# Kernel optimization log

Measured on AMD Instinct MI355X. Metric: run time of the kernel, lower is better.

## Reference

```python
import jax, jax.numpy as jnp
import numpy as np

T, H, I, E, K = 1024, 2048, 1408, 8, 2  # tokens, hidden, moe_intermediate, n_experts, top_k

def setup_inputs() -> dict:
    key = jax.random.key(0)
    k0, k1, k2, k3 = jax.random.split(key, 4)
    def w(k, shape, fan_in):
        return jax.random.normal(k, shape, jnp.float32) / np.float32(np.sqrt(fan_in))
    return {
        "hidden_states": jax.random.normal(k0, (T, H), jnp.float32),
        "gate_w": w(k1, (H, E), H),      # router: LiteLinear(H -> E), no bias
        "w1": w(k2, (E, H, I), H),        # experts_w1 [E, H, I]
        "w2": w(k3, (E, I, H), I),        # experts_w2 [E, I, H]
    }

def reference(hidden_states, gate_w, w1, w2):
    # Router: logits -> softmax -> top-k expert probabilities (no renorm; Qwen2MoE norm_topk_prob=False)
    router_logits = hidden_states @ gate_w                      # [T, E]
    probs = jax.nn.softmax(router_logits, axis=-1)              # [T, E]
    topk_vals, topk_idx = jax.lax.top_k(probs, K)               # [T, K]
    # Dense combine weights: zero except at the top-k experts of each token
    combine = jnp.sum(jax.nn.one_hot(topk_idx, E, dtype=probs.dtype) * topk_vals[..., None], axis=1)  # [T, E]
    # Expert MLP per source: down(silu(x @ w1)) — note: no gate/up split in this repo's fused_moe weights
    h = jnp.einsum('th,ehi->tei', hidden_states, w1)            # [T, E, I]
    y = jnp.einsum('tei,eih->teh', jax.nn.silu(h), w2)          # [T, E, H]
    return jnp.einsum('te,teh->th', combine, y)                 # [T, H]
```

## Files before the change

kernel.cpp:

```cpp
#include <hip/hip_runtime.h>
#include <hip/hip_fp16.h>

#define T_TOK 1024
#define H_DIM 2048
#define I_DIM 1408
#define N_EXP 8
#define TOPK  2

using f16x8 = __attribute__((ext_vector_type(8))) _Float16;
using f32x4 = __attribute__((ext_vector_type(4))) float;

#define BM 128
#define BN 64
#define BK 64
#define NTHR 512
#define MBLKS 8

#define WS_COUNTS      0
#define WS_BASES       256
#define WS_CURSORS     512
#define WS_TOPK_E      768
#define WS_TOPK_W      (768 + 8192)
#define WS_TOK_OF_SLOT 17408
#define WS_W_OF_SLOT   29696
#define WS_HACT        43008
#define WS_NEEDED      (43008 + 8650752)

__global__ void k_router(const float* __restrict__ X, const float* __restrict__ GW,
                         int* __restrict__ counts, int* __restrict__ topk_e,
                         float* __restrict__ topk_w) {
    int t = (blockIdx.x * blockDim.x + threadIdx.x) >> 6;
    int lane = threadIdx.x & 63;
    if (t >= T_TOK) return;
    float acc[N_EXP];
#pragma unroll
    for (int e = 0; e < N_EXP; ++e) acc[e] = 0.f;
    const float* xrow = X + (size_t)t * H_DIM;
    for (int h = lane; h < H_DIM; h += 64) {
        float x = xrow[h];
        const float* g = GW + (size_t)h * N_EXP;
#pragma unroll
        for (int e = 0; e < N_EXP; ++e) acc[e] = fmaf(x, g[e], acc[e]);
    }
#pragma unroll
    for (int off = 32; off > 0; off >>= 1) {
#pragma unroll
        for (int e = 0; e < N_EXP; ++e) acc[e] += __shfl_xor(acc[e], off, 64);
    }
    if (lane == 0) {
        float m = acc[0];
#pragma unroll
        for (int e = 1; e < N_EXP; ++e) m = fmaxf(m, acc[e]);
        float ex[N_EXP], s = 0.f;
#pragma unroll
        for (int e = 0; e < N_EXP; ++e) { ex[e] = expf(acc[e] - m); s += ex[e]; }
        float inv = 1.f / s;
        int e1 = 0;
#pragma unroll
        for (int e = 1; e < N_EXP; ++e) if (ex[e] > ex[e1]) e1 = e;
        int e2 = (e1 == 0) ? 1 : 0;
#pragma unroll
        for (int e = 0; e < N_EXP; ++e) if (e != e1 && ex[e] > ex[e2]) e2 = e;
        topk_e[t * 2 + 0] = e1;
        topk_e[t * 2 + 1] = e2;
        topk_w[t * 2 + 0] = ex[e1] * inv;
        topk_w[t * 2 + 1] = ex[e2] * inv;
        atomicAdd(&counts[e1], 1);
        atomicAdd(&counts[e2], 1);
    }
}

__global__ void k_prefix(const int* __restrict__ counts, int* __restrict__ bases,
                         int* __restrict__ cursors) {
    if (threadIdx.x == 0) {
        int b = 0;
        for (int e = 0; e < N_EXP; ++e) {
            bases[e] = b;
            b += ((counts[e] + BM - 1) / BM) * BM;
            cursors[e] = 0;
        }
    }
}

__global__ void k_scatter(const int* __restrict__ topk_e, const float* __restrict__ topk_w,
                          const int* __restrict__ bases, int* __restrict__ cursors,
                          int* __restrict__ tok_of_slot, float* __restrict__ w_of_slot) {
    int t = blockIdx.x * blockDim.x + threadIdx.x;
    if (t >= T_TOK) return;
    for (int j = 0; j < TOPK; ++j) {
        int e = topk_e[t * 2 + j];
        int pos = atomicAdd(&cursors[e], 1);
        int slot = bases[e] + pos;
        tok_of_slot[slot] = t;
        w_of_slot[slot] = topk_w[t * 2 + j];
    }
}


#define G_COMPUTE(buf)                                                          \
    do {                                                                        \
        _Pragma("unroll") for (int ks = 0; ks < 2; ++ks) {                      \
            f16x8 af[2], bf[2];                                                 \
            _Pragma("unroll") for (int ii = 0; ii < 2; ++ii) {                  \
                int r = wm + ii * 16 + rsel;                                    \
                af[ii] = *(const f16x8*)&As[buf][r][((kq + 4 * ks) ^ (r & 7)) * 8]; \
            }                                                                   \
            _Pragma("unroll") for (int jj = 0; jj < 2; ++jj) {                  \
                int r = wn + jj * 16 + rsel;                                    \
                bf[jj] = *(const f16x8*)&Bs[buf][r][((kq + 4 * ks) ^ (r & 7)) * 8]; \
            }                                                                   \
            _Pragma("unroll") for (int ii = 0; ii < 2; ++ii)                    \
                _Pragma("unroll") for (int jj = 0; jj < 2; ++jj)                \
                    acc[ii][jj] = __builtin_amdgcn_mfma_f32_16x16x32_f16(af[ii], bf[jj], acc[ii][jj], 0, 0, 0); \
        }                                                                       \
    } while (0)

#define G_DECODE(NB)                                \
    const int bi = blockIdx.x;                      \
    const int xcd = bi & 7;                         \
    const int kk = bi >> 3;                         \
    const int mblk = kk & (MBLKS - 1);              \
    const int P = xcd + 8 * (kk / MBLKS);           \
    const int e = P / (NB);                         \
    const int n = P % (NB);

__global__ __launch_bounds__(NTHR, 4) void k_gemm1(
    const float* __restrict__ X, const float* __restrict__ W1,
    const int* __restrict__ counts, const int* __restrict__ bases,
    const int* __restrict__ tok_of_slot, const float* __restrict__ w_of_slot,
    _Float16* __restrict__ hact) {
    __shared__ _Float16 As[2][BM][BK];
    __shared__ _Float16 Bs[2][BN][BK];

    G_DECODE(I_DIM / BN)
    const int cnt = counts[e];
    const int m0 = mblk * BM;
    if (m0 >= cnt) return;
    const int base = bases[e];
    const int n0 = n * BN;
    const int tid = threadIdx.x;

    const int ar = tid >> 2;
    const int ac2 = (tid & 3) * 2;
    const int r_eff = min(ar, cnt - m0 - 1);
    const float* arow = X + (size_t)tok_of_slot[base + m0 + r_eff] * H_DIM + (tid & 3) * 16;

    const int bn = tid & 63;
    const int bc = tid >> 6;
    const float* bcol = W1 + (size_t)e * (H_DIM * I_DIM) + (size_t)(bc * 8) * I_DIM + n0 + bn;

    const int wid = tid >> 6, lane = tid & 63;
    const int wm = (wid >> 1) * 32, wn = (wid & 1) * 32;
    const int rsel = lane & 15, kq = lane >> 4;

    f32x4 acc[2][2] = {};

    float4 aR0[4]; float bR0[8];
    float4 aR1[4]; float bR1[8];

#define LOAD1(aR, bR, k0)                                              \
    do {                                                               \
        aR[0] = *(const float4*)(arow + (k0));                         \
        aR[1] = *(const float4*)(arow + (k0) + 4);                     \
        aR[2] = *(const float4*)(arow + (k0) + 8);                     \
        aR[3] = *(const float4*)(arow + (k0) + 12);                    \
        const float* bp = bcol + (size_t)(k0) * I_DIM;                 \
        _Pragma("unroll") for (int j = 0; j < 8; ++j)                  \
            bR[j] = bp[(size_t)j * I_DIM];                             \
    } while (0)

#define STORE1(buf, aR, bR)                                            \
    do {                                                               \
        f16x8 p0, p1;                                                  \
        _Pragma("unroll") for (int j = 0; j < 4; ++j) {                \
            p0[j]     = (_Float16)aR[0][j];                            \
            p0[j + 4] = (_Float16)aR[1][j];                            \
            p1[j]     = (_Float16)aR[2][j];                            \
            p1[j + 4] = (_Float16)aR[3][j];                            \
        }                                                              \
        *(f16x8*)&As[buf][ar][((ac2) ^ (ar & 7)) * 8] = p0;            \
        *(f16x8*)&As[buf][ar][((ac2 + 1) ^ (ar & 7)) * 8] = p1;        \
        f16x8 q;                                                       \
        _Pragma("unroll") for (int j = 0; j < 8; ++j)                  \
            q[j] = (_Float16)bR[j];                                    \
        *(f16x8*)&Bs[buf][bn][(bc ^ (bn & 7)) * 8] = q;                \
    } while (0)

    const int KT = H_DIM / BK;
    LOAD1(aR0, bR0, 0);
    STORE1(0, aR0, bR0);
    LOAD1(aR0, bR0, BK);
    __syncthreads();
    for (int kt = 0; kt < KT; kt += 2) {
        if (kt + 2 < KT) LOAD1(aR1, bR1, (kt + 2) * BK);
        G_COMPUTE(0);
        if (kt + 1 < KT) STORE1(1, aR0, bR0);
        __syncthreads();
        if (kt + 3 < KT) LOAD1(aR0, bR0, (kt + 3) * BK);
        if (kt + 1 < KT) {
            G_COMPUTE(1);
            if (kt + 2 < KT) STORE1(0, aR1, bR1);
            __syncthreads();
        }
    }
#undef LOAD1
#undef STORE1

    const int rows = cnt - m0;
#pragma unroll
    for (int i = 0; i < 2; ++i) {
#pragma unroll
        for (int rg = 0; rg < 4; ++rg) {
            int r = wm + i * 16 + kq * 4 + rg;
            if (r < rows) {
                int slot = base + m0 + r;
                float w = w_of_slot[slot];
                _Float16* hrow = hact + (size_t)slot * I_DIM + n0;
#pragma unroll
                for (int j = 0; j < 2; ++j) {
                    float v = acc[i][j][rg];
                    hrow[wn + j * 16 + rsel] = (_Float16)(v / (1.f + expf(-v)) * w);
                }
            }
        }
    }
}

__global__ __launch_bounds__(NTHR, 4) void k_gemm2(
    const _Float16* __restrict__ hact, const float* __restrict__ W2,
    const int* __restrict__ counts, const int* __restrict__ bases,
    const int* __restrict__ tok_of_slot, float* __restrict__ out) {
    __shared__ _Float16 As[2][BM][BK];
    __shared__ _Float16 Bs[2][BN][BK];

    G_DECODE(H_DIM / BN)
    const int cnt = counts[e];
    const int m0 = mblk * BM;
    if (m0 >= cnt) return;
    const int base = bases[e];
    const int n0 = n * BN;
    const int tid = threadIdx.x;

    const int ar = tid >> 2;
    const int ac2 = (tid & 3) * 2;
    const int r_eff = min(ar, cnt - m0 - 1);
    const _Float16* arow = hact + (size_t)(base + m0 + r_eff) * I_DIM + (tid & 3) * 16;

    const int bn = tid & 63;
    const int bc = tid >> 6;
    const float* bcol = W2 + (size_t)e * (I_DIM * H_DIM) + (size_t)(bc * 8) * H_DIM + n0 + bn;

    const int wid = tid >> 6, lane = tid & 63;
    const int wm = (wid >> 1) * 32, wn = (wid & 1) * 32;
    const int rsel = lane & 15, kq = lane >> 4;

    f32x4 acc[2][2] = {};

    f16x8 aR0[2]; float bR0[8];
    f16x8 aR1[2]; float bR1[8];

#define LOAD2(aR, bR, k0)                                              \
    do {                                                               \
        aR[0] = *(const f16x8*)(arow + (k0));                          \
        aR[1] = *(const f16x8*)(arow + (k0) + 8);                      \
        const float* bp = bcol + (size_t)(k0) * H_DIM;                 \
        _Pragma("unroll") for (int j = 0; j < 8; ++j)                  \
            bR[j] = bp[(size_t)j * H_DIM];                             \
    } while (0)

#define STORE2(buf, aR, bR)                                            \
    do {                                                               \
        *(f16x8*)&As[buf][ar][((ac2) ^ (ar & 7)) * 8] = aR[0];         \
        *(f16x8*)&As[buf][ar][((ac2 + 1) ^ (ar & 7)) * 8] = aR[1];     \
        f16x8 q;                                                       \
        _Pragma("unroll") for (int j = 0; j < 8; ++j)                  \
            q[j] = (_Float16)bR[j];                                    \
        *(f16x8*)&Bs[buf][bn][(bc ^ (bn & 7)) * 8] = q;                \
    } while (0)

    const int KT = I_DIM / BK;
    LOAD2(aR0, bR0, 0);
    STORE2(0, aR0, bR0);
    LOAD2(aR0, bR0, BK);
    __syncthreads();
    for (int kt = 0; kt < KT; kt += 2) {
        if (kt + 2 < KT) LOAD2(aR1, bR1, (kt + 2) * BK);
        G_COMPUTE(0);
        if (kt + 1 < KT) STORE2(1, aR0, bR0);
        __syncthreads();
        if (kt + 3 < KT) LOAD2(aR0, bR0, (kt + 3) * BK);
        if (kt + 1 < KT) {
            G_COMPUTE(1);
            if (kt + 2 < KT) STORE2(0, aR1, bR1);
            __syncthreads();
        }
    }
#undef LOAD2
#undef STORE2

    const int rows = cnt - m0;
#pragma unroll
    for (int i = 0; i < 2; ++i) {
#pragma unroll
        for (int rg = 0; rg < 4; ++rg) {
            int r = wm + i * 16 + kq * 4 + rg;
            if (r < rows) {
                int slot = base + m0 + r;
                int tok = tok_of_slot[slot];
                float* orow = out + (size_t)tok * H_DIM + n0;
#pragma unroll
                for (int j = 0; j < 2; ++j)
                    atomicAdd(&orow[wn + j * 16 + rsel], acc[i][j][rg]);
            }
        }
    }
}

extern "C" void kernel_launch(void* const* d_in, const int* in_sizes, int n_in,
                              void* d_out, int out_size, void* d_ws, size_t ws_size,
                              hipStream_t stream) {
    const float* X  = (const float*)d_in[0];
    const float* GW = (const float*)d_in[1];
    const float* W1 = (const float*)d_in[2];
    const float* W2 = (const float*)d_in[3];
    float* out = (float*)d_out;
    char* ws = (char*)d_ws;
    if (ws_size < (size_t)WS_NEEDED) return;

    int*   counts      = (int*)(ws + WS_COUNTS);
    int*   bases       = (int*)(ws + WS_BASES);
    int*   cursors     = (int*)(ws + WS_CURSORS);
    int*   topk_e      = (int*)(ws + WS_TOPK_E);
    float* topk_w      = (float*)(ws + WS_TOPK_W);
    int*   tok_of_slot = (int*)(ws + WS_TOK_OF_SLOT);
    float* w_of_slot   = (float*)(ws + WS_W_OF_SLOT);
    _Float16* hact     = (_Float16*)(ws + WS_HACT);

    hipMemsetAsync(counts, 0, N_EXP * sizeof(int), stream);
    k_router<<<T_TOK / 4, 256, 0, stream>>>(X, GW, counts, topk_e, topk_w);
    k_prefix<<<1, 64, 0, stream>>>(counts, bases, cursors);
    k_scatter<<<T_TOK / 256, 256, 0, stream>>>(topk_e, topk_w, bases, cursors,
                                               tok_of_slot, w_of_slot);
    hipMemsetAsync(out, 0, (size_t)T_TOK * H_DIM * sizeof(float), stream);
    k_gemm1<<<8 * MBLKS * 22, NTHR, 0, stream>>>(
        X, W1, counts, bases, tok_of_slot, w_of_slot, hact);
    k_gemm2<<<8 * MBLKS * 32, NTHR, 0, stream>>>(
        hact, W2, counts, bases, tok_of_slot, out);
}
```

Measured before the change: 184.6 us.

## Use plain 3D grid, lighter barriers, and earlier output memset

Replaces the XCD-aware swizzled 1D block decode with a straightforward 3D grid (n tiles, m tiles, expert). It also replaces __syncthreads with an explicit lgkmcnt wait plus s_barrier, and moves the output memset to before the router. The 3D grid changes which blocks share an XCD L2, so the same weight tiles may be reused less within each L2 slice. The lighter barrier avoids waiting on outstanding global loads (vmcnt) at each sync, which could let the prefetches overlap more with compute.

```diff
diff --git a/kernel.cpp b/kernel.cpp
--- a/kernel.cpp
+++ b/kernel.cpp
@@ -14,7 +14,12 @@
 #define BN 64
 #define BK 64
 #define NTHR 512
-#define MBLKS 8
+
+#define BAR()                                                     \
+    do {                                                          \
+        asm volatile("s_waitcnt lgkmcnt(0)" ::: "memory");        \
+        __builtin_amdgcn_s_barrier();                             \
+    } while (0)
 
 #define WS_COUNTS      0
 #define WS_BASES       256
@@ -115,15 +120,6 @@
         }                                                                       \
     } while (0)
 
-#define G_DECODE(NB)                                \
-    const int bi = blockIdx.x;                      \
-    const int xcd = bi & 7;                         \
-    const int kk = bi >> 3;                         \
-    const int mblk = kk & (MBLKS - 1);              \
-    const int P = xcd + 8 * (kk / MBLKS);           \
-    const int e = P / (NB);                         \
-    const int n = P % (NB);
-
 __global__ __launch_bounds__(NTHR, 4) void k_gemm1(
     const float* __restrict__ X, const float* __restrict__ W1,
     const int* __restrict__ counts, const int* __restrict__ bases,
@@ -132,12 +128,12 @@
     __shared__ _Float16 As[2][BM][BK];
     __shared__ _Float16 Bs[2][BN][BK];
 
-    G_DECODE(I_DIM / BN)
+    const int e = blockIdx.z;
     const int cnt = counts[e];
-    const int m0 = mblk * BM;
+    const int m0 = blockIdx.y * BM;
     if (m0 >= cnt) return;
     const int base = bases[e];
-    const int n0 = n * BN;
+    const int n0 = blockIdx.x * BN;
     const int tid = threadIdx.x;
 
     const int ar = tid >> 2;
@@ -190,17 +186,17 @@
     LOAD1(aR0, bR0, 0);
     STORE1(0, aR0, bR0);
     LOAD1(aR0, bR0, BK);
-    __syncthreads();
+    BAR();
     for (int kt = 0; kt < KT; kt += 2) {
         if (kt + 2 < KT) LOAD1(aR1, bR1, (kt + 2) * BK);
         G_COMPUTE(0);
         if (kt + 1 < KT) STORE1(1, aR0, bR0);
-        __syncthreads();
+        BAR();
         if (kt + 3 < KT) LOAD1(aR0, bR0, (kt + 3) * BK);
         if (kt + 1 < KT) {
             G_COMPUTE(1);
             if (kt + 2 < KT) STORE1(0, aR1, bR1);
-            __syncthreads();
+            BAR();
         }
     }
 #undef LOAD1
@@ -233,12 +229,12 @@
     __shared__ _Float16 As[2][BM][BK];
     __shared__ _Float16 Bs[2][BN][BK];
 
-    G_DECODE(H_DIM / BN)
+    const int e = blockIdx.z;
     const int cnt = counts[e];
-    const int m0 = mblk * BM;
+    const int m0 = blockIdx.y * BM;
     if (m0 >= cnt) return;
     const int base = bases[e];
-    const int n0 = n * BN;
+    const int n0 = blockIdx.x * BN;
     const int tid = threadIdx.x;
 
     const int ar = tid >> 2;
@@ -282,17 +278,17 @@
     LOAD2(aR0, bR0, 0);
     STORE2(0, aR0, bR0);
     LOAD2(aR0, bR0, BK);
-    __syncthreads();
+    BAR();
     for (int kt = 0; kt < KT; kt += 2) {
         if (kt + 2 < KT) LOAD2(aR1, bR1, (kt + 2) * BK);
         G_COMPUTE(0);
         if (kt + 1 < KT) STORE2(1, aR0, bR0);
-        __syncthreads();
+        BAR();
         if (kt + 3 < KT) LOAD2(aR0, bR0, (kt + 3) * BK);
         if (kt + 1 < KT) {
             G_COMPUTE(1);
             if (kt + 2 < KT) STORE2(0, aR1, bR1);
-            __syncthreads();
+            BAR();
         }
     }
 #undef LOAD2
@@ -337,13 +333,13 @@
     _Float16* hact     = (_Float16*)(ws + WS_HACT);
 
     hipMemsetAsync(counts, 0, N_EXP * sizeof(int), stream);
+    hipMemsetAsync(out, 0, (size_t)T_TOK * H_DIM * sizeof(float), stream);
     k_router<<<T_TOK / 4, 256, 0, stream>>>(X, GW, counts, topk_e, topk_w);
     k_prefix<<<1, 64, 0, stream>>>(counts, bases, cursors);
     k_scatter<<<T_TOK / 256, 256, 0, stream>>>(topk_e, topk_w, bases, cursors,
                                                tok_of_slot, w_of_slot);
-    hipMemsetAsync(out, 0, (size_t)T_TOK * H_DIM * sizeof(float), stream);
-    k_gemm1<<<8 * MBLKS * 22, NTHR, 0, stream>>>(
+    k_gemm1<<<dim3(I_DIM / BN, T_TOK / BM, N_EXP), NTHR, 0, stream>>>(
         X, W1, counts, bases, tok_of_slot, w_of_slot, hact);
-    k_gemm2<<<8 * MBLKS * 32, NTHR, 0, stream>>>(
+    k_gemm2<<<dim3(H_DIM / BN, T_TOK / BM, N_EXP), NTHR, 0, stream>>>(
         hact, W2, counts, bases, tok_of_slot, out);
 }
```

Result: faster. 167.8 us (-9.1%).
